# Kernel optimization log

Measured on AMD Instinct MI355X. Metric: run time of the kernel, lower is better.

Reference implementation:

```python
import jax, jax.numpy as jnp
import numpy as np


def setup_inputs() -> dict:
    key = jax.random.key(0)
    ks = jax.random.split(key, 4)
    B, T, D, H = 64, 512, 512, 1024
    return {
        "x": jax.random.normal(ks[0], (B, T, D), dtype=jnp.float32),
        "kz": jax.random.normal(ks[1], (D, H), dtype=jnp.float32) * (1.0 / np.sqrt(D)),
        "kr": jax.random.normal(ks[2], (D, H), dtype=jnp.float32) * (1.0 / np.sqrt(D)),
        "kh": jax.random.normal(ks[3], (D, H), dtype=jnp.float32) * (1.0 / np.sqrt(D)),
        "mz": jnp.ones((H,), dtype=jnp.float32),
        "mr": jnp.ones((H,), dtype=jnp.float32),
        "br": jnp.zeros((H,), dtype=jnp.float32),
        "bz": jnp.zeros((H,), dtype=jnp.float32),
    }


def reference(x, kz, kr, kh, mz, mr, br, bz):
    B, T, D = x.shape
    H = kz.shape[1]
    # Precompute input projections for all timesteps (batched GEMMs),
    # identical math to per-step matmuls in the original cell.
    xz = jnp.einsum("btd,dh->bth", x, kz)  # [B,T,H]
    xr = jnp.einsum("btd,dh->bth", x, kr)
    xh = jnp.einsum("btd,dh->bth", x, kh)

    def step(h, inp):
        xz_t, xr_t, xh_t = inp  # each [B,H]
        r = jnp.tanh(xr_t + h * mr + br) + 1.0
        z = jax.nn.sigmoid(xz_t + h * mz + bz)
        h_new = z * h + (1.0 - z) * jnp.tanh(xh_t + r * h)
        return h_new, h_new

    h0 = jnp.zeros((B, H), dtype=x.dtype)
    # scan over time axis: move T to leading dim
    xs = (jnp.swapaxes(xz, 0, 1), jnp.swapaxes(xr, 0, 1), jnp.swapaxes(xh, 0, 1))
    _, ys = jax.lax.scan(step, h0, xs)  # ys: [T,B,H]
    return jnp.swapaxes(ys, 0, 1)  # [B,T,H]
```

## Files before the change

kernel.cpp:

```cpp
#include <hip/hip_runtime.h>
#include <hip/hip_bf16.h>
#include <math.h>


#define M_DIM 32768
#define K_DIM 512
#define H_DIM 1024
#define N3    3072

typedef _Float16 half8v __attribute__((ext_vector_type(8)));
typedef _Float16 half4v __attribute__((ext_vector_type(4)));
typedef float f32x4 __attribute__((ext_vector_type(4)));

__device__ __forceinline__ f32x4 mfma16(half8v a, half8v b, f32x4 c) {
    return __builtin_amdgcn_mfma_f32_16x16x32_f16(a, b, c, 0, 0, 0);
}

__device__ __forceinline__ void load_lds16(const void* g, void* l) {
    __builtin_amdgcn_global_load_lds(
        (const __attribute__((address_space(1))) void*)g,
        (__attribute__((address_space(3))) void*)l, 16, 0, 0);
}

__global__ __launch_bounds__(256) void convert_x(
    const float4* __restrict__ x4, half4v* __restrict__ hi4,
    half4v* __restrict__ lo4, int n4)
{
    int i = blockIdx.x * 256 + threadIdx.x;
    if (i >= n4) return;
    float4 v = x4[i];
    half4v h, lo;
    h.x = (_Float16)v.x; lo.x = (_Float16)(v.x - (float)h.x);
    h.y = (_Float16)v.y; lo.y = (_Float16)(v.y - (float)h.y);
    h.z = (_Float16)v.z; lo.z = (_Float16)(v.z - (float)h.z);
    h.w = (_Float16)v.w; lo.w = (_Float16)(v.w - (float)h.w);
    hi4[i] = h; lo4[i] = lo;
}

__global__ __launch_bounds__(256) void convert_wt(
    const float* __restrict__ kz, const float* __restrict__ kr,
    const float* __restrict__ kh, _Float16* __restrict__ wth,
    _Float16* __restrict__ wtl)
{
    int gid = blockIdx.x * 256 + threadIdx.x;
    int k = gid & (K_DIM - 1);
    int n = (gid >> 9) & (H_DIM - 1);
    int wsel = gid >> 19;
    const float* s = (wsel == 0) ? kz : ((wsel == 1) ? kr : kh);
    float v = s[(size_t)k * H_DIM + n];
    _Float16 h = (_Float16)v;
    wth[gid] = h;
    wtl[gid] = (_Float16)(v - (float)h);
}

__global__ __launch_bounds__(512, 2) void gemm_mfma_split(
    const _Float16* __restrict__ Ahi, const _Float16* __restrict__ Alo,
    const _Float16* __restrict__ Bthi, const _Float16* __restrict__ Btlo,
    float* __restrict__ XZ, float* __restrict__ XR, float* __restrict__ OUT)
{
    __shared__ _Float16 AT[2][256 * 64];
    __shared__ _Float16 BT[2][256 * 64];

    const int tid = threadIdx.x;
    const int w = tid >> 6, l = tid & 63;
    const int l15 = l & 15, quad = l >> 4;
    const int wr = w >> 2;
    const int wc = w & 3;

    const int nblk = blockIdx.x;
    const int swz = (nblk & 7) * 192 + (nblk >> 3);
    const int by = swz / 12;
    const int bx = swz - by * 12;
    const long m0 = (long)by * 256;
    const long n0 = (long)bx * 256;

    f32x4 acc[8][4] = {};

    const _Float16* gA[4]; const _Float16* gB[4];
    int lofs[4];
#pragma unroll
    for (int i = 0; i < 4; ++i) {
        const int s = i * 512 + tid;
        const int r = s >> 3;
        const int o2 = ((s & 7) ^ (r & 7)) << 4;
        const int part  = o2 >> 6;
        const int khalf = ((o2 >> 4) & 3) * 8;
        gA[i] = (part ? Alo : Ahi) + (m0 + r) * K_DIM + khalf;
        gB[i] = (part ? Btlo : Bthi) + (n0 + r) * K_DIM + khalf;
        lofs[i] = (i * 512 + (w << 6)) * 8;
    }

#pragma unroll
    for (int i = 0; i < 4; ++i) { load_lds16(gA[i], &AT[0][lofs[i]]); gA[i] += 32; }
#pragma unroll
    for (int i = 0; i < 4; ++i) { load_lds16(gB[i], &BT[0][lofs[i]]); gB[i] += 32; }
    asm volatile("s_waitcnt vmcnt(0)" ::: "memory");
    __builtin_amdgcn_s_barrier();

    for (int t = 0; t < 16; ++t) {
        const int cur = t & 1;
        const _Float16* at = &AT[cur][0];
        const _Float16* bt = &BT[cur][0];

        if (t + 1 < 16) {
            _Float16* an = &AT[cur ^ 1][0];
            _Float16* bn = &BT[cur ^ 1][0];
#pragma unroll
            for (int i = 0; i < 4; ++i) { load_lds16(gA[i], an + lofs[i]); gA[i] += 32; }
#pragma unroll
            for (int i = 0; i < 4; ++i) { load_lds16(gB[i], bn + lofs[i]); gB[i] += 32; }
        }

        half8v bfh[4], bfl[4];
#pragma unroll
        for (int ni = 0; ni < 4; ++ni) {
            const int r = wc * 64 + ni * 16 + l15;
            const int off = (quad ^ (r & 7)) * 8;
            bfh[ni] = *(const half8v*)&bt[r * 64 + off];
            bfl[ni] = *(const half8v*)&bt[r * 64 + (off ^ 32)];
        }
        half8v afh[4], afl[4];
#pragma unroll
        for (int mi = 0; mi < 4; ++mi) {
            const int r = wr * 128 + mi * 16 + l15;
            const int off = (quad ^ (r & 7)) * 8;
            afh[mi] = *(const half8v*)&at[r * 64 + off];
            afl[mi] = *(const half8v*)&at[r * 64 + (off ^ 32)];
        }
        __builtin_amdgcn_s_setprio(1);
#pragma unroll
        for (int mi = 0; mi < 4; ++mi)
#pragma unroll
            for (int ni = 0; ni < 4; ++ni)
                acc[mi][ni] = mfma16(afh[mi], bfh[ni], acc[mi][ni]);
#pragma unroll
        for (int mi = 0; mi < 4; ++mi)
#pragma unroll
            for (int ni = 0; ni < 4; ++ni)
                acc[mi][ni] = mfma16(afh[mi], bfl[ni], acc[mi][ni]);
#pragma unroll
        for (int mi = 0; mi < 4; ++mi)
#pragma unroll
            for (int ni = 0; ni < 4; ++ni)
                acc[mi][ni] = mfma16(afl[mi], bfh[ni], acc[mi][ni]);
        __builtin_amdgcn_s_setprio(0);

        half8v afh2[4], afl2[4];
#pragma unroll
        for (int mi = 0; mi < 4; ++mi) {
            const int r = wr * 128 + 64 + mi * 16 + l15;
            const int off = (quad ^ (r & 7)) * 8;
            afh2[mi] = *(const half8v*)&at[r * 64 + off];
            afl2[mi] = *(const half8v*)&at[r * 64 + (off ^ 32)];
        }
        __builtin_amdgcn_s_setprio(1);
#pragma unroll
        for (int mi = 0; mi < 4; ++mi)
#pragma unroll
            for (int ni = 0; ni < 4; ++ni)
                acc[4 + mi][ni] = mfma16(afh2[mi], bfh[ni], acc[4 + mi][ni]);
#pragma unroll
        for (int mi = 0; mi < 4; ++mi)
#pragma unroll
            for (int ni = 0; ni < 4; ++ni)
                acc[4 + mi][ni] = mfma16(afh2[mi], bfl[ni], acc[4 + mi][ni]);
#pragma unroll
        for (int mi = 0; mi < 4; ++mi)
#pragma unroll
            for (int ni = 0; ni < 4; ++ni)
                acc[4 + mi][ni] = mfma16(afl2[mi], bfh[ni], acc[4 + mi][ni]);
        __builtin_amdgcn_s_setprio(0);

        asm volatile("s_waitcnt vmcnt(0)" ::: "memory");
        __builtin_amdgcn_s_barrier();
    }

    float* dst = (bx < 4) ? XZ : ((bx < 8) ? XR : OUT);
    const long nl = (long)(bx & 3) * 256 + wc * 64 + l15;
#pragma unroll
    for (int mi = 0; mi < 8; ++mi) {
        const long m = m0 + wr * 128 + mi * 16 + quad * 4;
#pragma unroll
        for (int ni = 0; ni < 4; ++ni) {
            float* p = dst + m * H_DIM + nl + ni * 16;
#pragma unroll
            for (int i = 0; i < 4; ++i)
                p[(long)i * H_DIM] = acc[mi][ni][i];
        }
    }
}

#define BM 128
#define BN 128
#define BK 8
__global__ __launch_bounds__(256) void gemm_f32(
    const float* __restrict__ A, const float* __restrict__ B,
    float* __restrict__ C, int M, int N, int K)
{
    __shared__ float As[BK][BM];
    __shared__ float Bs[BK][BN];
    const int tid = threadIdx.x;
    const int bm = blockIdx.y * BM, bn = blockIdx.x * BN;
    const int tx = tid & 15, ty = tid >> 4;
    float acc[8][8];
#pragma unroll
    for (int i = 0; i < 8; i++)
#pragma unroll
        for (int j = 0; j < 8; j++) acc[i][j] = 0.f;
    const int a_row = tid >> 1, a_k = (tid & 1) * 4;
    const int b_row = tid >> 5, b_col = (tid & 31) * 4;
    const float* Aptr = A + (size_t)(bm + a_row) * K + a_k;
    const float* Bptr = B + (size_t)b_row * N + bn + b_col;
    for (int k0 = 0; k0 < K; k0 += BK) {
        float4 av = *(const float4*)(Aptr + k0);
        float4 bv = *(const float4*)(Bptr + (size_t)k0 * N);
        As[a_k + 0][a_row] = av.x; As[a_k + 1][a_row] = av.y;
        As[a_k + 2][a_row] = av.z; As[a_k + 3][a_row] = av.w;
        *(float4*)&Bs[b_row][b_col] = bv;
        __syncthreads();
#pragma unroll
        for (int kk = 0; kk < BK; kk++) {
            float4 a0 = *(const float4*)&As[kk][ty * 8];
            float4 a1 = *(const float4*)&As[kk][ty * 8 + 4];
            float4 b0 = *(const float4*)&Bs[kk][tx * 8];
            float4 b1 = *(const float4*)&Bs[kk][tx * 8 + 4];
            float a[8] = {a0.x, a0.y, a0.z, a0.w, a1.x, a1.y, a1.z, a1.w};
            float b[8] = {b0.x, b0.y, b0.z, b0.w, b1.x, b1.y, b1.z, b1.w};
#pragma unroll
            for (int i = 0; i < 8; i++)
#pragma unroll
                for (int j = 0; j < 8; j++)
                    acc[i][j] = fmaf(a[i], b[j], acc[i][j]);
        }
        __syncthreads();
    }
    float* Cptr = C + (size_t)(bm + ty * 8) * N + bn + tx * 8;
#pragma unroll
    for (int i = 0; i < 8; i++) {
        float4 c0 = {acc[i][0], acc[i][1], acc[i][2], acc[i][3]};
        float4 c1 = {acc[i][4], acc[i][5], acc[i][6], acc[i][7]};
        *(float4*)(Cptr + (size_t)i * N)     = c0;
        *(float4*)(Cptr + (size_t)i * N + 4) = c1;
    }
}

__device__ __forceinline__ float vrcp_nr(float d) {
    float r = __builtin_amdgcn_rcpf(d);
    return r * fmaf(-d, r, 2.0f);
}

__global__ __launch_bounds__(256) void scan_kernel(
    const float* __restrict__ XZ, const float* __restrict__ XR,
    float* __restrict__ OUT,
    const float* __restrict__ mz, const float* __restrict__ mr,
    const float* __restrict__ br, const float* __restrict__ bz)
{
    const int gid = blockIdx.x * blockDim.x + threadIdx.x;
    const int b = gid >> 10;
    const int h = gid & (H_DIM - 1);

    const float mzK = -mz[h];
    const float mrK = -2.0f * mr[h];
    const float bzK = -bz[h];
    const float brK = -2.0f * br[h];
    float hs = 0.f;
    size_t idx = (size_t)b * 512 * H_DIM + h;

    float cz[16], cr[16], ch[16];
#pragma unroll
    for (int j = 0; j < 16; ++j) {
        cz[j] = bzK - XZ[idx + (size_t)j * H_DIM];
        cr[j] = fmaf(-2.0f, XR[idx + (size_t)j * H_DIM], brK);
        ch[j] = -2.0f * OUT[idx + (size_t)j * H_DIM];
    }
    for (int t0 = 0; t0 < 512; t0 += 16) {
        float nz[16], nr[16], nh[16];
        const bool more = (t0 + 16) < 512;
        const size_t nidx = idx + 16ul * H_DIM;
        if (more) {
#pragma unroll
            for (int j = 0; j < 16; ++j) {
                nz[j] = XZ[nidx + (size_t)j * H_DIM];
                nr[j] = XR[nidx + (size_t)j * H_DIM];
                nh[j] = OUT[nidx + (size_t)j * H_DIM];
            }
        }
#pragma unroll
        for (int j = 0; j < 16; ++j) {
            const float u1   = fmaf(hs, mrK, cr[j]);
            const float uz   = fmaf(hs, mzK, cz[j]);
            const float hsK2 = -4.0f * hs;
            const float e1 = __expf(u1);
            const float s1 = vrcp_nr(e1 + 1.0f);
            const float ez = __expf(uz);
            const float sz = vrcp_nr(ez + 1.0f);
            const float u2 = fmaf(s1, hsK2, ch[j]);
            const float e2 = __expf(u2);
            const float s2 = vrcp_nr(e2 + 1.0f);
            const float th = fmaf(2.0f, s2, -1.0f);
            const float hn = fmaf(sz, hs - th, th);
            OUT[idx + (size_t)j * H_DIM] = hn;
            hs = hn;
        }
        idx = nidx;
        if (more) {
#pragma unroll
            for (int j = 0; j < 16; ++j) {
                cz[j] = bzK - nz[j];
                cr[j] = fmaf(-2.0f, nr[j], brK);
                ch[j] = -2.0f * nh[j];
            }
        }
    }
}

extern "C" void kernel_launch(void* const* d_in, const int* in_sizes, int n_in,
                              void* d_out, int out_size, void* d_ws, size_t ws_size,
                              hipStream_t stream) {
    const float* x  = (const float*)d_in[0];
    const float* kz = (const float*)d_in[1];
    const float* kr = (const float*)d_in[2];
    const float* kh = (const float*)d_in[3];
    const float* mz = (const float*)d_in[4];
    const float* mr = (const float*)d_in[5];
    const float* br = (const float*)d_in[6];
    const float* bz = (const float*)d_in[7];
    float* out = (float*)d_out;

    char* ws = (char*)d_ws;
    float* XZ = (float*)ws;
    float* XR = (float*)(ws + 134217728ul);
    _Float16* XHI = (_Float16*)(ws + 268435456ul);
    _Float16* XLO = (_Float16*)(ws + 301989888ul);
    _Float16* WTH = (_Float16*)(ws + 335544320ul);
    _Float16* WTL = (_Float16*)(ws + 338690048ul);
    const size_t need = 341835776ul;

    if (ws_size >= need) {
        int n4 = M_DIM * K_DIM / 4;
        convert_x<<<n4 / 256, 256, 0, stream>>>(
            (const float4*)x, (half4v*)XHI, (half4v*)XLO, n4);
        convert_wt<<<(3 * H_DIM * K_DIM) / 256, 256, 0, stream>>>(
            kz, kr, kh, WTH, WTL);
        gemm_mfma_split<<<1536, 512, 0, stream>>>(
            XHI, XLO, WTH, WTL, XZ, XR, out);
    } else {
        dim3 grid(H_DIM / BN, M_DIM / BM);
        gemm_f32<<<grid, 256, 0, stream>>>(x, kz, XZ,  M_DIM, H_DIM, K_DIM);
        gemm_f32<<<grid, 256, 0, stream>>>(x, kr, XR,  M_DIM, H_DIM, K_DIM);
        gemm_f32<<<grid, 256, 0, stream>>>(x, kh, out, M_DIM, H_DIM, K_DIM);
    }

    scan_kernel<<<(64 * H_DIM) / 256, 256, 0, stream>>>(
        XZ, XR, out, mz, mr, br, bz);
}
```

Measured before the change: 586.8 us.

## Interleave split global prefetches with LDS reads and MFMA phases in GEMM loop

Splits each K-step of the projection GEMM into four phases. Each phase issues a quarter of the next tile's global-to-LDS loads, reads a slice of fragments from LDS, then runs a block of MFMAs, with barriers and sched_barrier fences between phases. The aim is to spread memory traffic across compute and keep LDS reads and MFMAs in a fixed order, in the style of a ping-pong schedule. It adds several workgroup barriers per iteration, which may stall waves and cost more than the overlap gains.

```diff
diff --git a/kernel.cpp b/kernel.cpp
--- a/kernel.cpp
+++ b/kernel.cpp
@@ -101,38 +101,59 @@
         const int cur = t & 1;
         const _Float16* at = &AT[cur][0];
         const _Float16* bt = &BT[cur][0];
-
-        if (t + 1 < 16) {
-            _Float16* an = &AT[cur ^ 1][0];
-            _Float16* bn = &BT[cur ^ 1][0];
-#pragma unroll
-            for (int i = 0; i < 4; ++i) { load_lds16(gA[i], an + lofs[i]); gA[i] += 32; }
-#pragma unroll
-            for (int i = 0; i < 4; ++i) { load_lds16(gB[i], bn + lofs[i]); gB[i] += 32; }
-        }
-
-        half8v bfh[4], bfl[4];
+        _Float16* an = &AT[cur ^ 1][0];
+        _Float16* bn = &BT[cur ^ 1][0];
+        const bool pf = (t + 1) < 16;
+
+        if (pf) {
+            load_lds16(gA[0], an + lofs[0]); gA[0] += 32;
+            load_lds16(gA[1], an + lofs[1]); gA[1] += 32;
+        }
+        half8v bfh[4], bfl[4], afh[4], afl[4];
 #pragma unroll
         for (int ni = 0; ni < 4; ++ni) {
             const int r = wc * 64 + ni * 16 + l15;
             const int off = (quad ^ (r & 7)) * 8;
             bfh[ni] = *(const half8v*)&bt[r * 64 + off];
-            bfl[ni] = *(const half8v*)&bt[r * 64 + (off ^ 32)];
-        }
-        half8v afh[4], afl[4];
+        }
 #pragma unroll
         for (int mi = 0; mi < 4; ++mi) {
             const int r = wr * 128 + mi * 16 + l15;
             const int off = (quad ^ (r & 7)) * 8;
             afh[mi] = *(const half8v*)&at[r * 64 + off];
+        }
+        __builtin_amdgcn_s_barrier();
+        asm volatile("s_waitcnt lgkmcnt(0)" ::: "memory");
+        __builtin_amdgcn_sched_barrier(0);
+        __builtin_amdgcn_s_setprio(1);
+#pragma unroll
+        for (int mi = 0; mi < 4; ++mi)
+#pragma unroll
+            for (int ni = 0; ni < 4; ++ni)
+                acc[mi][ni] = mfma16(afh[mi], bfh[ni], acc[mi][ni]);
+        __builtin_amdgcn_s_setprio(0);
+        __builtin_amdgcn_s_barrier();
+
+        if (pf) {
+            load_lds16(gA[2], an + lofs[2]); gA[2] += 32;
+            load_lds16(gA[3], an + lofs[3]); gA[3] += 32;
+        }
+#pragma unroll
+        for (int ni = 0; ni < 4; ++ni) {
+            const int r = wc * 64 + ni * 16 + l15;
+            const int off = (quad ^ (r & 7)) * 8;
+            bfl[ni] = *(const half8v*)&bt[r * 64 + (off ^ 32)];
+        }
+#pragma unroll
+        for (int mi = 0; mi < 4; ++mi) {
+            const int r = wr * 128 + mi * 16 + l15;
+            const int off = (quad ^ (r & 7)) * 8;
             afl[mi] = *(const half8v*)&at[r * 64 + (off ^ 32)];
         }
+        __builtin_amdgcn_s_barrier();
+        asm volatile("s_waitcnt lgkmcnt(0)" ::: "memory");
+        __builtin_amdgcn_sched_barrier(0);
         __builtin_amdgcn_s_setprio(1);
-#pragma unroll
-        for (int mi = 0; mi < 4; ++mi)
-#pragma unroll
-            for (int ni = 0; ni < 4; ++ni)
-                acc[mi][ni] = mfma16(afh[mi], bfh[ni], acc[mi][ni]);
 #pragma unroll
         for (int mi = 0; mi < 4; ++mi)
 #pragma unroll
@@ -144,21 +165,45 @@
             for (int ni = 0; ni < 4; ++ni)
                 acc[mi][ni] = mfma16(afl[mi], bfh[ni], acc[mi][ni]);
         __builtin_amdgcn_s_setprio(0);
-
+        __builtin_amdgcn_s_barrier();
+
+        if (pf) {
+            load_lds16(gB[0], bn + lofs[0]); gB[0] += 32;
+            load_lds16(gB[1], bn + lofs[1]); gB[1] += 32;
+        }
         half8v afh2[4], afl2[4];
 #pragma unroll
         for (int mi = 0; mi < 4; ++mi) {
             const int r = wr * 128 + 64 + mi * 16 + l15;
             const int off = (quad ^ (r & 7)) * 8;
             afh2[mi] = *(const half8v*)&at[r * 64 + off];
+        }
+        __builtin_amdgcn_s_barrier();
+        asm volatile("s_waitcnt lgkmcnt(0)" ::: "memory");
+        __builtin_amdgcn_sched_barrier(0);
+        __builtin_amdgcn_s_setprio(1);
+#pragma unroll
+        for (int mi = 0; mi < 4; ++mi)
+#pragma unroll
+            for (int ni = 0; ni < 4; ++ni)
+                acc[4 + mi][ni] = mfma16(afh2[mi], bfh[ni], acc[4 + mi][ni]);
+        __builtin_amdgcn_s_setprio(0);
+        __builtin_amdgcn_s_barrier();
+
+        if (pf) {
+            load_lds16(gB[2], bn + lofs[2]); gB[2] += 32;
+            load_lds16(gB[3], bn + lofs[3]); gB[3] += 32;
+        }
+#pragma unroll
+        for (int mi = 0; mi < 4; ++mi) {
+            const int r = wr * 128 + 64 + mi * 16 + l15;
+            const int off = (quad ^ (r & 7)) * 8;
             afl2[mi] = *(const half8v*)&at[r * 64 + (off ^ 32)];
         }
+        __builtin_amdgcn_s_barrier();
+        asm volatile("s_waitcnt lgkmcnt(0)" ::: "memory");
+        __builtin_amdgcn_sched_barrier(0);
         __builtin_amdgcn_s_setprio(1);
-#pragma unroll
-        for (int mi = 0; mi < 4; ++mi)
-#pragma unroll
-            for (int ni = 0; ni < 4; ++ni)
-                acc[4 + mi][ni] = mfma16(afh2[mi], bfh[ni], acc[4 + mi][ni]);
 #pragma unroll
         for (int mi = 0; mi < 4; ++mi)
 #pragma unroll
@@ -170,7 +215,6 @@
             for (int ni = 0; ni < 4; ++ni)
                 acc[4 + mi][ni] = mfma16(afl2[mi], bfh[ni], acc[4 + mi][ni]);
         __builtin_amdgcn_s_setprio(0);
-
         asm volatile("s_waitcnt vmcnt(0)" ::: "memory");
         __builtin_amdgcn_s_barrier();
     }
```

After: 622.6 us. +6.1%, slower.
